# Performance work log

Measured on AMD Instinct MI355X. Metric: run time of the kernel, lower is better.

## Reference

```python
import jax, jax.numpy as jnp
import numpy as np

D_MODEL = 1024
HEADS = 4
DK = 1024          # key_dim = d_model * expand_k
DV = 2048          # value_dim = d_model * expand_v
HDK = DK // HEADS  # 256
HDV = DV // HEADS  # 512
LOW_RANK = 16
CHUNK = 64
GATE_NORM = 16.0
EPS = 1e-5


def setup_inputs() -> dict:
    key = jax.random.key(0)
    ks = jax.random.split(key, 10)
    gain = 2.0 ** (-2.5)

    def xavier(k, shape):  # shape = (fan_in, fan_out); stored as [in, out]
        lim = gain * np.sqrt(6.0 / (shape[0] + shape[1]))
        return jax.random.uniform(k, shape, jnp.float32, -lim, lim)

    return {
        'x': jax.random.normal(ks[0], (2, 2048, D_MODEL), jnp.float32),
        'Wq': xavier(ks[1], (D_MODEL, DK)),
        'Wk': xavier(ks[2], (D_MODEL, DK)),
        'Wv': xavier(ks[3], (D_MODEL, DV)),
        'Wg': xavier(ks[4], (D_MODEL, DV)),
        'Wgk1': xavier(ks[5], (D_MODEL, LOW_RANK)),
        'Wgk2': xavier(ks[6], (LOW_RANK, DK)),
        'bgk2': jnp.zeros((DK,), jnp.float32),
        'Wo': xavier(ks[7], (DV, D_MODEL)),
        'rms_w': jnp.ones((HDV,), jnp.float32),
    }


def _gla_chunked(q, k, v, g):
    """Gated linear attention: S_t = exp(g_t) (*) S_{t-1} + k_t^T v_t;  o_t = scale * q_t @ S_t.
    q,k,g: [B,H,T,HDK]; v: [B,H,T,HDV]. Chunk-parallel formulation, scan over chunks."""
    B, H, T, _ = q.shape
    NC = T // CHUNK
    scale = HDK ** -0.5

    def to_chunks(t, d):  # [B,H,T,d] -> [NC,B,H,CHUNK,d]
        return t.reshape(B, H, NC, CHUNK, d).transpose(2, 0, 1, 3, 4)

    qc = to_chunks(q, HDK)
    kc = to_chunks(k, HDK)
    vc = to_chunks(v, HDV)
    bc = jnp.cumsum(to_chunks(g, HDK), axis=-2)  # inclusive log-decay within chunk
    mask = jnp.tril(jnp.ones((CHUNK, CHUNK), bool))

    def step(S, inp):
        qb, kb, vb, bb = inp                       # [B,H,C,HDK/HDV]
        qg = qb * jnp.exp(bb) * scale              # queries decayed to chunk start
        kd = kb * jnp.exp(-bb)                     # keys un-decayed (intra)
        A = jnp.einsum('bhtd,bhsd->bhts', qg, kd)  # intra-chunk scores
        A = jnp.where(mask, A, 0.0)
        o = jnp.einsum('bhts,bhsv->bhtv', A, vb) + jnp.einsum('bhtd,bhdv->bhtv', qg, S)
        b_last = bb[:, :, -1:, :]                  # [B,H,1,HDK]
        kg = kb * jnp.exp(b_last - bb)             # keys decayed to chunk end
        S = S * jnp.exp(b_last[:, :, 0, :])[..., None] + jnp.einsum('bhtd,bhtv->bhdv', kg, vb)
        return S, o

    S0 = jnp.zeros((B, H, HDK, HDV), q.dtype)
    _, o = jax.lax.scan(step, S0, (qc, kc, vc, bc))  # o: [NC,B,H,C,HDV]
    return o.transpose(1, 2, 0, 3, 4).reshape(B, H, T, HDV)


def reference(x, Wq, Wk, Wv, Wg, Wgk1, Wgk2, bgk2, Wo, rms_w):
    B, T, _ = x.shape
    q = (x @ Wq).reshape(B, T, HEADS, HDK).transpose(0, 2, 1, 3)
    k = (x @ Wk).reshape(B, T, HEADS, HDK).transpose(0, 2, 1, 3)
    v = (x @ Wv).reshape(B, T, HEADS, HDV).transpose(0, 2, 1, 3)
    gk = (x @ Wgk1) @ Wgk2 + bgk2                       # low-rank gate logits
    g = jax.nn.log_sigmoid(gk.astype(jnp.float32)) / GATE_NORM
    g = g.reshape(B, T, HEADS, HDK).transpose(0, 2, 1, 3)

    o = _gla_chunked(q, k, v, g)                        # [B,H,T,HDV]
    o = o.transpose(0, 2, 1, 3)                         # [B,T,H,HDV]
    o = o * jax.lax.rsqrt(jnp.mean(o * o, axis=-1, keepdims=True) + EPS) * rms_w
    o = o.reshape(B, T, HEADS * HDV)
    o = o * jax.nn.silu(x @ Wg)
    return o @ Wo
```

## Files before the change

### kernel.cpp

```cpp
#include <hip/hip_runtime.h>
#include <hip/hip_bf16.h>
#include <math.h>

#define TOK  4096
#define DM   1024
#define DKC  1024
#define DVC  2048
#define NH   4
#define HDK_ 256
#define HDV_ 512
#define NCH  32
#define CHK  64

typedef __attribute__((ext_vector_type(8))) short bf16x8;
typedef __attribute__((ext_vector_type(4))) float f32x4;

__device__ inline float bf2f(short s) {
    unsigned int b = ((unsigned int)(unsigned short)s) << 16;
    return __uint_as_float(b);
}
__device__ inline short f2bf_bits(float f) {
    __hip_bfloat16 h = __float2bfloat16(f);
    return *reinterpret_cast<short*>(&h);
}

__device__ __forceinline__ void gl_lds16(const void* g, void* l) {
    __builtin_amdgcn_global_load_lds((const __attribute__((address_space(1))) void*)g,
                                     (__attribute__((address_space(3))) void*)l, 16, 0, 0);
}

__global__ __launch_bounds__(256) void prep_all(const float* __restrict__ Wq,
                                                const float* __restrict__ Wk,
                                                const float* __restrict__ Wv,
                                                const float* __restrict__ Wg,
                                                const float* __restrict__ Wo,
                                                __hip_bfloat16* __restrict__ WtAll,
                                                __hip_bfloat16* __restrict__ WtO,
                                                const float* __restrict__ x,
                                                const float* __restrict__ W1,
                                                const float* __restrict__ W2,
                                                const float* __restrict__ b2,
                                                __hip_bfloat16* __restrict__ xb,
                                                float* __restrict__ g) {
    const int bid = blockIdx.x;
    const int tid = threadIdx.x;
    if (bid < 8192) {
        __shared__ float tile[32][33];
        const float* W; __hip_bfloat16* Wt; int K, N, r;
        if (bid < 1024)      { W = Wq; Wt = WtAll;               K = 1024; N = 1024; r = bid; }
        else if (bid < 2048) { W = Wk; Wt = WtAll + 1024 * 1024; K = 1024; N = 1024; r = bid - 1024; }
        else if (bid < 4096) { W = Wv; Wt = WtAll + 2048 * 1024; K = 1024; N = 2048; r = bid - 2048; }
        else if (bid < 6144) { W = Wg; Wt = WtAll + 4096 * 1024; K = 1024; N = 2048; r = bid - 4096; }
        else                 { W = Wo; Wt = WtO;                 K = 2048; N = 1024; r = bid - 6144; }
        const int ncols = N >> 5;
        const int n0 = (r % ncols) * 32, k0 = (r / ncols) * 32;
        const int tx = tid & 31, ty = tid >> 5;
#pragma unroll
        for (int i = 0; i < 32; i += 8)
            tile[ty + i][tx] = W[(size_t)(k0 + ty + i) * N + n0 + tx];
        __syncthreads();
#pragma unroll
        for (int i = 0; i < 32; i += 8)
            Wt[(size_t)(n0 + ty + i) * K + k0 + tx] = __float2bfloat16(tile[tx][ty + i]);
    } else {
        __shared__ float xl[1024];
        __shared__ float red[16][17];
        __shared__ float t1l[16];
        const int t = bid - 8192;
        float4 xv = *reinterpret_cast<const float4*>(&x[(size_t)t * DM + tid * 4]);
        *reinterpret_cast<float4*>(&xl[tid * 4]) = xv;
        short4 xs;
        xs.x = f2bf_bits(xv.x); xs.y = f2bf_bits(xv.y);
        xs.z = f2bf_bits(xv.z); xs.w = f2bf_bits(xv.w);
        *reinterpret_cast<short4*>((short*)xb + (size_t)t * DM + tid * 4) = xs;
        __syncthreads();
        const int o = tid & 15, p = tid >> 4;
        float s = 0.f;
#pragma unroll 8
        for (int m = 0; m < 64; ++m) {
            int kk = p * 64 + m;
            s += xl[kk] * W1[kk * 16 + o];
        }
        red[p][o] = s;
        __syncthreads();
        if (tid < 16) {
            float tot = 0.f;
#pragma unroll
            for (int pp = 0; pp < 16; ++pp) tot += red[pp][tid];
            t1l[tid] = tot;
        }
        __syncthreads();
#pragma unroll
        for (int j = 0; j < 4; ++j) {
            int c = tid + j * 256;
            float acc = b2[c];
#pragma unroll
            for (int r2 = 0; r2 < 16; ++r2) acc += t1l[r2] * W2[r2 * 1024 + c];
            float ls = fminf(acc, 0.f) - log1pf(expf(-fabsf(acc)));
            g[(size_t)t * DKC + c] = ls * (1.f / 16.f);
        }
    }
}

__global__ __launch_bounds__(512) void gemm256(const __hip_bfloat16* __restrict__ A,
                                               const __hip_bfloat16* __restrict__ Wt,
                                               __hip_bfloat16* __restrict__ qo,
                                               __hip_bfloat16* __restrict__ ko,
                                               __hip_bfloat16* __restrict__ vT,
                                               __hip_bfloat16* __restrict__ xgo) {
    __shared__ __align__(16) short SM[9 * 8192];
    const int K = 1024, NT = 16;
    const int tid = threadIdx.x;
    const int wave = tid >> 6, lane = tid & 63;
    const int wr = wave >> 2;
    const int wc = wave & 3;
    const int hc = wc >> 1;
    const int l15 = lane & 15, kb = lane >> 4;
    const int m0 = blockIdx.y * 128, n0 = blockIdx.x * 256;

    const bool isV = (n0 >= 2048 && n0 < 4096);
    __hip_bfloat16* dst = nullptr; int ldd = 0, nloc0 = 0;
    if (n0 < 1024)       { dst = qo;  ldd = 1024; nloc0 = n0; }
    else if (n0 < 2048)  { dst = ko;  ldd = 1024; nloc0 = n0 - 1024; }
    else if (n0 >= 4096) { dst = xgo; ldd = 2048; nloc0 = n0 - 4096; }

    f32x4 acc[4][4];
#pragma unroll
    for (int mf = 0; mf < 4; ++mf)
#pragma unroll
        for (int nf = 0; nf < 4; ++nf) acc[mf][nf] = (f32x4){0.f, 0.f, 0.f, 0.f};

    auto stage_unit = [&](int u) {
        int tk = u / 3, p = u % 3;
        int slot = u % 9;
#pragma unroll
        for (int j = 0; j < 2; ++j) {
            int row = (wave * 2 + j) * 8 + (lane >> 3);
            int srcg = (lane & 7) ^ (row & 7);
            const __hip_bfloat16* src =
                (p == 0) ? &A[(size_t)(m0 + row) * K + tk * 64 + srcg * 8]
                         : &Wt[(size_t)(n0 + (p - 1) * 128 + row) * K + tk * 64 + srcg * 8];
            gl_lds16(src, &SM[slot * 8192 + (wave * 2 + j) * 512]);
        }
    };

    for (int u = 0; u <= 5; ++u) stage_unit(u);

    const int ULAST = 3 * NT - 1;
    for (int t = 0; t < NT; ++t) {
        if (t < NT - 1) asm volatile("s_waitcnt vmcnt(6)" ::: "memory");
        else            asm volatile("s_waitcnt vmcnt(0)" ::: "memory");
        __builtin_amdgcn_sched_barrier(0);
        __builtin_amdgcn_s_barrier();

        if (3 * t + 6 <= ULAST) stage_unit(3 * t + 6);
        if (3 * t + 7 <= ULAST) stage_unit(3 * t + 7);
        if (3 * t + 8 <= ULAST) stage_unit(3 * t + 8);
        __builtin_amdgcn_sched_barrier(0);

        const short* Abase = &SM[((3 * t) % 9) * 8192];
        const short* Bbase = &SM[((3 * t + 1 + hc) % 9) * 8192];

        bf16x8 a0[4], b0[4], a1[4], b1[4];
#pragma unroll
        for (int mf = 0; mf < 4; ++mf) {
            int row = wr * 64 + mf * 16 + l15;
            a0[mf] = *reinterpret_cast<const bf16x8*>(&Abase[row * 64 + (kb ^ (row & 7)) * 8]);
        }
#pragma unroll
        for (int nf = 0; nf < 4; ++nf) {
            int row = (wc & 1) * 64 + nf * 16 + l15;
            b0[nf] = *reinterpret_cast<const bf16x8*>(&Bbase[row * 64 + (kb ^ (row & 7)) * 8]);
        }
        __builtin_amdgcn_sched_barrier(0);
#pragma unroll
        for (int mf = 0; mf < 4; ++mf) {
            int row = wr * 64 + mf * 16 + l15;
            a1[mf] = *reinterpret_cast<const bf16x8*>(&Abase[row * 64 + ((4 + kb) ^ (row & 7)) * 8]);
        }
#pragma unroll
        for (int nf = 0; nf < 4; ++nf) {
            int row = (wc & 1) * 64 + nf * 16 + l15;
            b1[nf] = *reinterpret_cast<const bf16x8*>(&Bbase[row * 64 + ((4 + kb) ^ (row & 7)) * 8]);
        }
        __builtin_amdgcn_sched_barrier(0);
        asm volatile("s_waitcnt lgkmcnt(8)" ::: "memory");
        __builtin_amdgcn_sched_barrier(0);
        __builtin_amdgcn_s_setprio(1);
#pragma unroll
        for (int mf = 0; mf < 4; ++mf)
#pragma unroll
            for (int nf = 0; nf < 4; ++nf)
                acc[mf][nf] = __builtin_amdgcn_mfma_f32_16x16x32_bf16(a0[mf], b0[nf], acc[mf][nf], 0, 0, 0);
        __builtin_amdgcn_s_setprio(0);
        asm volatile("s_waitcnt lgkmcnt(0)" ::: "memory");
        __builtin_amdgcn_sched_barrier(0);
        __builtin_amdgcn_s_setprio(1);
#pragma unroll
        for (int mf = 0; mf < 4; ++mf)
#pragma unroll
            for (int nf = 0; nf < 4; ++nf)
                acc[mf][nf] = __builtin_amdgcn_mfma_f32_16x16x32_bf16(a1[mf], b1[nf], acc[mf][nf], 0, 0, 0);
        __builtin_amdgcn_s_setprio(0);
    }

    if (!isV) {
#pragma unroll
        for (int mf = 0; mf < 4; ++mf)
#pragma unroll
            for (int nf = 0; nf < 4; ++nf)
#pragma unroll
                for (int r = 0; r < 4; ++r)
                    dst[(size_t)(m0 + wr * 64 + mf * 16 + kb * 4 + r) * ldd +
                        nloc0 + wc * 64 + nf * 16 + l15] = __float2bfloat16(acc[mf][nf][r]);
    } else {
        __syncthreads();
        short* Cl = SM;
#pragma unroll
        for (int mf = 0; mf < 4; ++mf)
#pragma unroll
            for (int nf = 0; nf < 4; ++nf)
#pragma unroll
                for (int r = 0; r < 4; ++r) {
                    int trow = wr * 64 + mf * 16 + kb * 4 + r;
                    int vcol = wc * 64 + nf * 16 + l15;
                    Cl[vcol * 132 + trow] = f2bf_bits(acc[mf][nf][r]);
                }
        __syncthreads();
        const int vcg0 = n0 - 2048;
        const int bh = (m0 >> 11) * NH + (vcg0 >> 9);
        const int vl0 = vcg0 & 511;
        const int tl0 = m0 & 2047;
        short* vTs = (short*)vT;
#pragma unroll
        for (int it = 0; it < 8; ++it) {
            int idx = tid + it * 512;
            int row = idx >> 4;
            int c8 = (idx & 15) * 8;
            bf16x8 vv = *reinterpret_cast<const bf16x8*>(&Cl[row * 132 + c8]);
            *reinterpret_cast<bf16x8*>(
                &vTs[((size_t)(bh * 512 + vl0 + row)) * 2048 + tl0 + c8]) = vv;
        }
    }
}

__global__ __launch_bounds__(256) void gemm_bf16(const __hip_bfloat16* __restrict__ A,
                                                 const __hip_bfloat16* __restrict__ Wt,
                                                 float* __restrict__ C,
                                                 int M, int N, int K) {
    __shared__ __align__(16) short Buf[2][2][128 * 64];
    const int tid = threadIdx.x;
    const int wave = tid >> 6, lane = tid & 63;
    const int wr = wave >> 1, wc = wave & 1;
    const int m0 = blockIdx.y * 128, n0 = blockIdx.x * 128;
    const int l15 = lane & 15, kb = lane >> 4;
    const int lr8 = lane >> 3, lc8 = (lane & 7) * 8;
    const int NT = K >> 6;

    f32x4 acc[4][4];
#pragma unroll
    for (int mf = 0; mf < 4; ++mf)
#pragma unroll
        for (int nf = 0; nf < 4; ++nf) acc[mf][nf] = (f32x4){0.f, 0.f, 0.f, 0.f};

#define STAGE_G(kt, bi)                                                          \
    {                                                                            \
        int k0s = (kt) * 64;                                                     \
        _Pragma("unroll")                                                        \
        for (int j = 0; j < 4; ++j) {                                            \
            int inst = wave * 4 + j;                                             \
            int r = inst * 8 + lr8;                                              \
            gl_lds16(&A[(size_t)(m0 + r) * K + k0s + lc8], &Buf[bi][0][inst * 512]); \
            gl_lds16(&Wt[(size_t)(n0 + r) * K + k0s + lc8], &Buf[bi][1][inst * 512]); \
        }                                                                        \
    }

    STAGE_G(0, 0);
    STAGE_G(1, 1);

    for (int t = 0; t < NT; ++t) {
        if (t + 1 < NT) asm volatile("s_waitcnt vmcnt(8)" ::: "memory");
        else            asm volatile("s_waitcnt vmcnt(0)" ::: "memory");
        __builtin_amdgcn_sched_barrier(0);
        __builtin_amdgcn_s_barrier();
        const short* Ab = Buf[t & 1][0];
        const short* Bb = Buf[t & 1][1];
        bf16x8 a0[4], b0[4], a1[4], b1[4];
#pragma unroll
        for (int mf = 0; mf < 4; ++mf)
            a0[mf] = *reinterpret_cast<const bf16x8*>(&Ab[(wr * 64 + mf * 16 + l15) * 64 + kb * 8]);
#pragma unroll
        for (int nf = 0; nf < 4; ++nf)
            b0[nf] = *reinterpret_cast<const bf16x8*>(&Bb[(wc * 64 + nf * 16 + l15) * 64 + kb * 8]);
        __builtin_amdgcn_sched_barrier(0);
#pragma unroll
        for (int mf = 0; mf < 4; ++mf)
            a1[mf] = *reinterpret_cast<const bf16x8*>(&Ab[(wr * 64 + mf * 16 + l15) * 64 + 32 + kb * 8]);
#pragma unroll
        for (int nf = 0; nf < 4; ++nf)
            b1[nf] = *reinterpret_cast<const bf16x8*>(&Bb[(wc * 64 + nf * 16 + l15) * 64 + 32 + kb * 8]);
        __builtin_amdgcn_sched_barrier(0);
        asm volatile("s_waitcnt lgkmcnt(8)" ::: "memory");
        __builtin_amdgcn_sched_barrier(0);
#pragma unroll
        for (int mf = 0; mf < 4; ++mf)
#pragma unroll
            for (int nf = 0; nf < 4; ++nf)
                acc[mf][nf] = __builtin_amdgcn_mfma_f32_16x16x32_bf16(a0[mf], b0[nf], acc[mf][nf], 0, 0, 0);
        asm volatile("s_waitcnt lgkmcnt(0)" ::: "memory");
        __builtin_amdgcn_sched_barrier(0);
#pragma unroll
        for (int mf = 0; mf < 4; ++mf)
#pragma unroll
            for (int nf = 0; nf < 4; ++nf)
                acc[mf][nf] = __builtin_amdgcn_mfma_f32_16x16x32_bf16(a1[mf], b1[nf], acc[mf][nf], 0, 0, 0);
        __builtin_amdgcn_sched_barrier(0);
        __builtin_amdgcn_s_barrier();
        if (t + 2 < NT) STAGE_G(t + 2, t & 1);
    }
#undef STAGE_G

#pragma unroll
    for (int mf = 0; mf < 4; ++mf)
#pragma unroll
        for (int nf = 0; nf < 4; ++nf)
#pragma unroll
            for (int r = 0; r < 4; ++r)
                C[(size_t)(m0 + wr * 64 + mf * 16 + kb * 4 + r) * N + n0 + wc * 64 + nf * 16 + l15] =
                    acc[mf][nf][r];
}

__global__ __launch_bounds__(256) void gla_chunk(const __hip_bfloat16* __restrict__ qb,
                                                 const __hip_bfloat16* __restrict__ kb,
                                                 const __hip_bfloat16* __restrict__ vT,
                                                 const float* __restrict__ g,
                                                 __hip_bfloat16* __restrict__ qg,
                                                 __hip_bfloat16* __restrict__ kgT,
                                                 __hip_bfloat16* __restrict__ o1,
                                                 float* __restrict__ dlast) {
    __shared__ __align__(16) short SM[36864];
    short* qg_l = SM;
    short* kd_l = SM + 16384;
    short* V_l  = SM;
    short* Am_l = SM + 32768;

    const int chunk = blockIdx.x, bh = blockIdx.y;
    const int b = bh >> 2, h = bh & 3;
    const int t0 = b * 2048 + chunk * 64;
    const int tt0 = chunk * 64;
    const int tid = threadIdx.x;
    const float scale = 0.0625f;

    {
        const int d = tid;
        const float* gcol = g + (size_t)t0 * DKC + h * HDK_ + d;
        const __hip_bfloat16* qcol = qb + (size_t)t0 * DKC + h * HDK_ + d;
        const __hip_bfloat16* kcol = kb + (size_t)t0 * DKC + h * HDK_ + d;
        float run = 0.f;
#pragma unroll
        for (int i = 0; i < 64; ++i) run += gcol[(size_t)i * DKC];
        const float ebl = expf(run);
        dlast[((size_t)bh * NCH + chunk) * HDK_ + d] = ebl;

        bf16x8 kreg[8];
        run = 0.f;
#pragma unroll
        for (int i = 0; i < 64; ++i) {
            run += gcol[(size_t)i * DKC];
            float eb = expf(run);
            float qv = __bfloat162float(qcol[(size_t)i * DKC]) * eb * scale;
            float kdv = __bfloat162float(kcol[(size_t)i * DKC]) * expf(-run);
            qg[(size_t)(t0 + i) * DKC + h * HDK_ + d] = __float2bfloat16(qv);
            int bq = ((i * 512 + d * 2) ^ ((i & 7) << 4)) >> 1;
            qg_l[bq] = f2bf_bits(qv);
            kd_l[bq] = f2bf_bits(kdv);
            kreg[i >> 3][i & 7] = f2bf_bits(kdv * ebl);
        }
        __hip_bfloat16* kdst = kgT + ((size_t)(bh * HDK_ + d)) * 2048 + chunk * 64;
#pragma unroll
        for (int j = 0; j < 8; ++j)
            *reinterpret_cast<bf16x8*>(&kdst[j * 8]) = kreg[j];
    }
    __syncthreads();

    const int wv = tid >> 6, lane = tid & 63;
    const int l15 = lane & 15, kb_ = lane >> 4;

    {
        f32x4 accA[4];
#pragma unroll
        for (int sf = 0; sf < 4; ++sf) accA[sf] = (f32x4){0.f, 0.f, 0.f, 0.f};
        const int trow = wv * 16 + l15;
#pragma unroll
        for (int ks = 0; ks < 8; ++ks) {
            bf16x8 af = *reinterpret_cast<const bf16x8*>(
                &qg_l[((trow * 512 + (ks * 32 + kb_ * 8) * 2) ^ ((trow & 7) << 4)) >> 1]);
#pragma unroll
            for (int sf = 0; sf < 4; ++sf) {
                int srow = sf * 16 + l15;
                bf16x8 bfr = *reinterpret_cast<const bf16x8*>(
                    &kd_l[((srow * 512 + (ks * 32 + kb_ * 8) * 2) ^ ((srow & 7) << 4)) >> 1]);
                accA[sf] = __builtin_amdgcn_mfma_f32_16x16x32_bf16(af, bfr, accA[sf], 0, 0, 0);
            }
        }
#pragma unroll
        for (int sf = 0; sf < 4; ++sf)
#pragma unroll
            for (int r = 0; r < 4; ++r) {
                int t = wv * 16 + kb_ * 4 + r, s = sf * 16 + l15;
                float val = (t >= s) ? accA[sf][r] : 0.f;
                Am_l[((t * 128 + s * 2) ^ ((t & 7) << 4)) >> 1] = f2bf_bits(val);
            }
    }
    __syncthreads();

    {
        const int lr8 = lane >> 3, slot = lane & 7;
#pragma unroll
        for (int i8 = 0; i8 < 16; ++i8) {
            int vrow0 = wv * 128 + i8 * 8;
            const __hip_bfloat16* src =
                &vT[((size_t)bh * 512 + vrow0 + lr8) * 2048 + tt0 + (slot ^ (lr8 & 7)) * 8];
            gl_lds16(src, &V_l[vrow0 * 64]);
        }
    }
    __syncthreads();

    {
        f32x4 accO[4][8];
#pragma unroll
        for (int tf = 0; tf < 4; ++tf)
#pragma unroll
            for (int vf = 0; vf < 8; ++vf) accO[tf][vf] = (f32x4){0.f, 0.f, 0.f, 0.f};
#pragma unroll
        for (int kk = 0; kk < 2; ++kk) {
            bf16x8 af[4];
#pragma unroll
            for (int tf = 0; tf < 4; ++tf) {
                int row = tf * 16 + l15;
                af[tf] = *reinterpret_cast<const bf16x8*>(
                    &Am_l[((row * 128 + (kk * 32 + kb_ * 8) * 2) ^ ((row & 7) << 4)) >> 1]);
            }
#pragma unroll
            for (int vf = 0; vf < 8; ++vf) {
                int rv = wv * 128 + vf * 16 + l15;
                bf16x8 bfr = *reinterpret_cast<const bf16x8*>(
                    &V_l[((rv * 128 + (kk * 32 + kb_ * 8) * 2) ^ ((rv & 7) << 4)) >> 1]);
#pragma unroll
                for (int tf = 0; tf < 4; ++tf)
                    accO[tf][vf] = __builtin_amdgcn_mfma_f32_16x16x32_bf16(af[tf], bfr, accO[tf][vf], 0, 0, 0);
            }
        }
#pragma unroll
        for (int tf = 0; tf < 4; ++tf)
#pragma unroll
            for (int vf = 0; vf < 8; ++vf)
#pragma unroll
                for (int r = 0; r < 4; ++r) {
                    int t = tf * 16 + kb_ * 4 + r;
                    int vv = wv * 128 + vf * 16 + l15;
                    o1[(size_t)(t0 + t) * DVC + h * HDV_ + vv] = __float2bfloat16(accO[tf][vf][r]);
                }
    }
}

__global__ __launch_bounds__(256) void u_pass(const __hip_bfloat16* __restrict__ vT,
                                              const __hip_bfloat16* __restrict__ kgT,
                                              __hip_bfloat16* __restrict__ U) {
    __shared__ __align__(16) short Av[128 * 64];
    __shared__ __align__(16) short Bv[128 * 64];
    const int bx = blockIdx.x, c = blockIdx.y, bh = blockIdx.z;
    const int vc0 = (bx >> 1) * 128, d0 = (bx & 1) * 128;
    const int tid = threadIdx.x;
    const int wave = tid >> 6, lane = tid & 63;
    const int wr = wave >> 1, wc = wave & 1;
    const int l15 = lane & 15, kb = lane >> 4;
    const int lr8 = lane >> 3, lc8 = (lane & 7) * 8;

#pragma unroll
    for (int j = 0; j < 4; ++j) {
        int inst = wave * 4 + j;
        int r = inst * 8 + lr8;
        gl_lds16(&vT[((size_t)bh * 512 + vc0 + r) * 2048 + c * 64 + lc8], &Av[inst * 512]);
        gl_lds16(&kgT[((size_t)bh * HDK_ + d0 + r) * 2048 + c * 64 + lc8], &Bv[inst * 512]);
    }
    __syncthreads();

    f32x4 acc[4][4];
#pragma unroll
    for (int mf = 0; mf < 4; ++mf)
#pragma unroll
        for (int nf = 0; nf < 4; ++nf) acc[mf][nf] = (f32x4){0.f, 0.f, 0.f, 0.f};
#pragma unroll
    for (int kk = 0; kk < 2; ++kk) {
        bf16x8 af[4], bfr[4];
#pragma unroll
        for (int mf = 0; mf < 4; ++mf)
            af[mf] = *reinterpret_cast<const bf16x8*>(&Av[(wr * 64 + mf * 16 + l15) * 64 + kk * 32 + kb * 8]);
#pragma unroll
        for (int nf = 0; nf < 4; ++nf)
            bfr[nf] = *reinterpret_cast<const bf16x8*>(&Bv[(wc * 64 + nf * 16 + l15) * 64 + kk * 32 + kb * 8]);
#pragma unroll
        for (int mf = 0; mf < 4; ++mf)
#pragma unroll
            for (int nf = 0; nf < 4; ++nf)
                acc[mf][nf] = __builtin_amdgcn_mfma_f32_16x16x32_bf16(af[mf], bfr[nf], acc[mf][nf], 0, 0, 0);
    }
    const size_t Ub = ((size_t)bh * NCH + c) * 131072;
#pragma unroll
    for (int mf = 0; mf < 4; ++mf)
#pragma unroll
        for (int nf = 0; nf < 4; ++nf)
#pragma unroll
            for (int r = 0; r < 4; ++r) {
                int vc = vc0 + wr * 64 + mf * 16 + kb * 4 + r;
                int d = d0 + wc * 64 + nf * 16 + l15;
                U[Ub + (size_t)vc * 256 + d] = __float2bfloat16(acc[mf][nf][r]);
            }
}

__global__ __launch_bounds__(256) void scan_pass(__hip_bfloat16* __restrict__ U,
                                                 const float* __restrict__ dlast) {
    int gid = blockIdx.x * 256 + threadIdx.x;
    int bh = gid >> 14;
    int rem = gid & 16383;
    int vc = rem >> 5;
    int dg = rem & 31;
    float S[8];
#pragma unroll
    for (int j = 0; j < 8; ++j) S[j] = 0.f;
    size_t base = (size_t)bh * NCH * 131072 + (size_t)vc * 256 + dg * 8;
    for (int c = 0; c < NCH; ++c) {
        __hip_bfloat16* p = U + base + (size_t)c * 131072;
        bf16x8 u = *reinterpret_cast<bf16x8*>(p);
        const float* dl = &dlast[((size_t)bh * NCH + c) * HDK_ + dg * 8];
        float4 e0 = *reinterpret_cast<const float4*>(dl);
        float4 e1 = *reinterpret_cast<const float4*>(dl + 4);
        float e[8] = {e0.x, e0.y, e0.z, e0.w, e1.x, e1.y, e1.z, e1.w};
        bf16x8 outv;
#pragma unroll
        for (int j = 0; j < 8; ++j) {
            outv[j] = f2bf_bits(S[j]);
            S[j] = S[j] * e[j] + bf2f(u[j]);
        }
        *reinterpret_cast<bf16x8*>(p) = outv;
    }
}

__global__ __launch_bounds__(256) void o_pass(const __hip_bfloat16* __restrict__ qg,
                                              const __hip_bfloat16* __restrict__ U,
                                              const __hip_bfloat16* __restrict__ o1,
                                              __hip_bfloat16* __restrict__ o2) {
    __shared__ __align__(16) char smem[64 * 132 * 4];
    short* Av = (short*)smem;
    short* Bv = (short*)smem + 128 * 64;
    float* oT = (float*)smem;
    const int vt = blockIdx.x, c = blockIdx.y, bh = blockIdx.z;
    const int b = bh >> 2, h = bh & 3;
    const int vc0 = vt * 128;
    const int t0 = b * 2048 + c * 64;
    const int tid = threadIdx.x;
    const int wave = tid >> 6, lane = tid & 63;
    const int wr = wave >> 1, wc = wave & 1;
    const int l15 = lane & 15, kb = lane >> 4;
    const int lr8 = lane >> 3, lc8 = (lane & 7) * 8;
    const size_t Ub = ((size_t)bh * NCH + c) * 131072;

    f32x4 acc[4][2];
#pragma unroll
    for (int mf = 0; mf < 4; ++mf)
#pragma unroll
        for (int nf = 0; nf < 2; ++nf) acc[mf][nf] = (f32x4){0.f, 0.f, 0.f, 0.f};

    for (int ks = 0; ks < 4; ++ks) {
        const int d0 = ks * 64;
#pragma unroll
        for (int j = 0; j < 4; ++j) {
            int inst = wave * 4 + j;
            int r = inst * 8 + lr8;
            gl_lds16(&U[Ub + (size_t)(vc0 + r) * 256 + d0 + lc8], &Av[inst * 512]);
        }
#pragma unroll
        for (int j = 0; j < 2; ++j) {
            int inst = wave * 2 + j;
            int r = inst * 8 + lr8;
            gl_lds16(&qg[(size_t)(t0 + r) * DKC + h * HDK_ + d0 + lc8], &Bv[inst * 512]);
        }
        __syncthreads();
#pragma unroll
        for (int kk = 0; kk < 2; ++kk) {
            bf16x8 af[4], bfr[2];
#pragma unroll
            for (int mf = 0; mf < 4; ++mf)
                af[mf] = *reinterpret_cast<const bf16x8*>(&Av[(wr * 64 + mf * 16 + l15) * 64 + kk * 32 + kb * 8]);
#pragma unroll
            for (int nf = 0; nf < 2; ++nf)
                bfr[nf] = *reinterpret_cast<const bf16x8*>(&Bv[(wc * 32 + nf * 16 + l15) * 64 + kk * 32 + kb * 8]);
#pragma unroll
            for (int mf = 0; mf < 4; ++mf)
#pragma unroll
                for (int nf = 0; nf < 2; ++nf)
                    acc[mf][nf] = __builtin_amdgcn_mfma_f32_16x16x32_bf16(af[mf], bfr[nf], acc[mf][nf], 0, 0, 0);
        }
        __syncthreads();
    }
#pragma unroll
    for (int mf = 0; mf < 4; ++mf)
#pragma unroll
        for (int nf = 0; nf < 2; ++nf)
#pragma unroll
            for (int r = 0; r < 4; ++r)
                oT[(wc * 32 + nf * 16 + l15) * 132 + wr * 64 + mf * 16 + kb * 4 + r] = acc[mf][nf][r];
    __syncthreads();
#pragma unroll
    for (int j = 0; j < 4; ++j) {
        int t = (tid >> 4) + j * 16;
        int vc8 = (tid & 15) * 8;
        float4 a0 = *reinterpret_cast<const float4*>(&oT[t * 132 + vc8]);
        float4 a1 = *reinterpret_cast<const float4*>(&oT[t * 132 + vc8 + 4]);
        size_t oi = (size_t)(t0 + t) * DVC + h * HDV_ + vc0 + vc8;
        bf16x8 iv = *reinterpret_cast<const bf16x8*>(&o1[oi]);
        bf16x8 outv;
        outv[0] = f2bf_bits(a0.x + bf2f(iv[0]));
        outv[1] = f2bf_bits(a0.y + bf2f(iv[1]));
        outv[2] = f2bf_bits(a0.z + bf2f(iv[2]));
        outv[3] = f2bf_bits(a0.w + bf2f(iv[3]));
        outv[4] = f2bf_bits(a1.x + bf2f(iv[4]));
        outv[5] = f2bf_bits(a1.y + bf2f(iv[5]));
        outv[6] = f2bf_bits(a1.z + bf2f(iv[6]));
        outv[7] = f2bf_bits(a1.w + bf2f(iv[7]));
        *reinterpret_cast<bf16x8*>((__hip_bfloat16*)o2 + oi) = outv;
    }
}

__global__ __launch_bounds__(256) void rms_gate(const __hip_bfloat16* __restrict__ o2,
                                                const __hip_bfloat16* __restrict__ xg,
                                                const float* __restrict__ rms_w,
                                                __hip_bfloat16* __restrict__ gated) {
    __shared__ float wsum[4];
    const int th = blockIdx.x;
    const int t = th >> 2, h = th & 3;
    const int tid = threadIdx.x;
    const size_t base = (size_t)t * DVC + h * HDV_;
    short2 ov = reinterpret_cast<const short2*>((const short*)o2 + base)[tid];
    float v0 = bf2f(ov.x), v1 = bf2f(ov.y);
    float s = v0 * v0 + v1 * v1;
#pragma unroll
    for (int off = 32; off >= 1; off >>= 1) s += __shfl_down(s, off, 64);
    if ((tid & 63) == 0) wsum[tid >> 6] = s;
    __syncthreads();
    float tot = wsum[0] + wsum[1] + wsum[2] + wsum[3];
    float rms = rsqrtf(tot * (1.f / 512.f) + 1e-5f);
    short2 gv = reinterpret_cast<const short2*>((const short*)xg + base)[tid];
    float g0 = bf2f(gv.x), g1 = bf2f(gv.y);
    float s0 = g0 / (1.f + expf(-g0));
    float s1 = g1 / (1.f + expf(-g1));
    float2 w = reinterpret_cast<const float2*>(rms_w)[tid];
    short2 outp;
    outp.x = f2bf_bits(v0 * rms * w.x * s0);
    outp.y = f2bf_bits(v1 * rms * w.y * s1);
    reinterpret_cast<short2*>((short*)gated + base)[tid] = outp;
}

extern "C" void kernel_launch(void* const* d_in, const int* in_sizes, int n_in,
                              void* d_out, int out_size, void* d_ws, size_t ws_size,
                              hipStream_t stream) {
    const float* x    = (const float*)d_in[0];
    const float* Wq   = (const float*)d_in[1];
    const float* Wk   = (const float*)d_in[2];
    const float* Wv   = (const float*)d_in[3];
    const float* Wg   = (const float*)d_in[4];
    const float* Wgk1 = (const float*)d_in[5];
    const float* Wgk2 = (const float*)d_in[6];
    const float* bgk2 = (const float*)d_in[7];
    const float* Wo   = (const float*)d_in[8];
    const float* rmsw = (const float*)d_in[9];
    float* out = (float*)d_out;
    float* ws = (float*)d_ws;

    const size_t M1 = 1ull << 20;
    __hip_bfloat16* xb    = (__hip_bfloat16*)ws;
    __hip_bfloat16* WtAll = (__hip_bfloat16*)(ws + 2 * M1);
    __hip_bfloat16* q_b   = (__hip_bfloat16*)(ws + 5 * M1);
    __hip_bfloat16* k_b   = (__hip_bfloat16*)(ws + 7 * M1);
    float*          g     = ws + 13 * M1;
    __hip_bfloat16* U     = (__hip_bfloat16*)ws;
    __hip_bfloat16* xg_b  = (__hip_bfloat16*)(ws + 17 * M1);
    __hip_bfloat16* qgb   = (__hip_bfloat16*)(ws + 21 * M1);
    __hip_bfloat16* kgT   = (__hip_bfloat16*)(ws + 23 * M1);
    __hip_bfloat16* vT    = (__hip_bfloat16*)(ws + 25 * M1);
    __hip_bfloat16* o1    = (__hip_bfloat16*)(ws + 29 * M1);
    __hip_bfloat16* o2    = (__hip_bfloat16*)(ws + 33 * M1);
    float*          dlast = ws + 37 * M1 + 65536;
    __hip_bfloat16* WtO   = (__hip_bfloat16*)(ws + 38 * M1);
    __hip_bfloat16* gated = (__hip_bfloat16*)(ws + 25 * M1);

    prep_all<<<12288, 256, 0, stream>>>(Wq, Wk, Wv, Wg, Wo, WtAll, WtO,
                                        x, Wgk1, Wgk2, bgk2, xb, g);

    gemm256<<<dim3(24, 32), 512, 0, stream>>>(xb, WtAll, q_b, k_b, vT, xg_b);

    gla_chunk<<<dim3(NCH, 8), 256, 0, stream>>>(q_b, k_b, vT, g, qgb, kgT, o1, dlast);

    u_pass<<<dim3(8, NCH, 8), 256, 0, stream>>>(vT, kgT, U);
    scan_pass<<<512, 256, 0, stream>>>(U, dlast);
    o_pass<<<dim3(4, NCH, 8), 256, 0, stream>>>(qgb, U, o1, o2);

    rms_gate<<<TOK * NH, 256, 0, stream>>>(o2, xg_b, rmsw, gated);
    gemm_bf16<<<dim3(8, 32), 256, 0, stream>>>(gated, WtO, out, TOK, DM, DVC);
}
```

Baseline: 238.0 us.

## Fuse chunk state-update GEMM into gla_chunk and drop kgT round-trip

```diff
diff --git a/kernel.cpp b/kernel.cpp
--- a/kernel.cpp
+++ b/kernel.cpp
@@ -335,14 +335,15 @@
                                                  const __hip_bfloat16* __restrict__ vT,
                                                  const float* __restrict__ g,
                                                  __hip_bfloat16* __restrict__ qg,
-                                                 __hip_bfloat16* __restrict__ kgT,
+                                                 __hip_bfloat16* __restrict__ U,
                                                  __hip_bfloat16* __restrict__ o1,
                                                  float* __restrict__ dlast) {
-    __shared__ __align__(16) short SM[36864];
+    __shared__ __align__(16) short SM[53248];
     short* qg_l = SM;
     short* kd_l = SM + 16384;
     short* V_l  = SM;
-    short* Am_l = SM + 32768;
+    short* kg_l = SM + 32768;
+    short* Am_l = SM + 49152;
 
     const int chunk = blockIdx.x, bh = blockIdx.y;
     const int b = bh >> 2, h = bh & 3;
@@ -376,10 +377,9 @@
             kd_l[bq] = f2bf_bits(kdv);
             kreg[i >> 3][i & 7] = f2bf_bits(kdv * ebl);
         }
-        __hip_bfloat16* kdst = kgT + ((size_t)(bh * HDK_ + d)) * 2048 + chunk * 64;
 #pragma unroll
         for (int j = 0; j < 8; ++j)
-            *reinterpret_cast<bf16x8*>(&kdst[j * 8]) = kreg[j];
+            *reinterpret_cast<bf16x8*>(&kg_l[d * 64 + ((j ^ (d & 7)) * 8)]) = kreg[j];
     }
     __syncthreads();
 
@@ -462,61 +462,48 @@
                     o1[(size_t)(t0 + t) * DVC + h * HDV_ + vv] = __float2bfloat16(accO[tf][vf][r]);
                 }
     }
-}
-
-__global__ __launch_bounds__(256) void u_pass(const __hip_bfloat16* __restrict__ vT,
-                                              const __hip_bfloat16* __restrict__ kgT,
-                                              __hip_bfloat16* __restrict__ U) {
-    __shared__ __align__(16) short Av[128 * 64];
-    __shared__ __align__(16) short Bv[128 * 64];
-    const int bx = blockIdx.x, c = blockIdx.y, bh = blockIdx.z;
-    const int vc0 = (bx >> 1) * 128, d0 = (bx & 1) * 128;
-    const int tid = threadIdx.x;
-    const int wave = tid >> 6, lane = tid & 63;
-    const int wr = wave >> 1, wc = wave & 1;
-    const int l15 = lane & 15, kb = lane >> 4;
-    const int lr8 = lane >> 3, lc8 = (lane & 7) * 8;
-
-#pragma unroll
-    for (int j = 0; j < 4; ++j) {
-        int inst = wave * 4 + j;
-        int r = inst * 8 + lr8;
-        gl_lds16(&vT[((size_t)bh * 512 + vc0 + r) * 2048 + c * 64 + lc8], &Av[inst * 512]);
-        gl_lds16(&kgT[((size_t)bh * HDK_ + d0 + r) * 2048 + c * 64 + lc8], &Bv[inst * 512]);
-    }
-    __syncthreads();
-
-    f32x4 acc[4][4];
-#pragma unroll
-    for (int mf = 0; mf < 4; ++mf)
-#pragma unroll
-        for (int nf = 0; nf < 4; ++nf) acc[mf][nf] = (f32x4){0.f, 0.f, 0.f, 0.f};
-#pragma unroll
-    for (int kk = 0; kk < 2; ++kk) {
-        bf16x8 af[4], bfr[4];
-#pragma unroll
-        for (int mf = 0; mf < 4; ++mf)
-            af[mf] = *reinterpret_cast<const bf16x8*>(&Av[(wr * 64 + mf * 16 + l15) * 64 + kk * 32 + kb * 8]);
-#pragma unroll
-        for (int nf = 0; nf < 4; ++nf)
-            bfr[nf] = *reinterpret_cast<const bf16x8*>(&Bv[(wc * 64 + nf * 16 + l15) * 64 + kk * 32 + kb * 8]);
-#pragma unroll
-        for (int mf = 0; mf < 4; ++mf)
-#pragma unroll
-            for (int nf = 0; nf < 4; ++nf)
-                acc[mf][nf] = __builtin_amdgcn_mfma_f32_16x16x32_bf16(af[mf], bfr[nf], acc[mf][nf], 0, 0, 0);
-    }
-    const size_t Ub = ((size_t)bh * NCH + c) * 131072;
-#pragma unroll
-    for (int mf = 0; mf < 4; ++mf)
-#pragma unroll
-        for (int nf = 0; nf < 4; ++nf)
-#pragma unroll
-            for (int r = 0; r < 4; ++r) {
-                int vc = vc0 + wr * 64 + mf * 16 + kb * 4 + r;
-                int d = d0 + wc * 64 + nf * 16 + l15;
-                U[Ub + (size_t)vc * 256 + d] = __float2bfloat16(acc[mf][nf][r]);
+
+    {
+        const size_t Ub = ((size_t)bh * NCH + chunk) * 131072;
+        for (int d0 = 0; d0 < 256; d0 += 64) {
+            f32x4 accU[8][4];
+#pragma unroll
+            for (int vf = 0; vf < 8; ++vf)
+#pragma unroll
+                for (int nf = 0; nf < 4; ++nf) accU[vf][nf] = (f32x4){0.f, 0.f, 0.f, 0.f};
+#pragma unroll
+            for (int kk = 0; kk < 2; ++kk) {
+                bf16x8 av[8], bv[4];
+#pragma unroll
+                for (int vf = 0; vf < 8; ++vf) {
+                    int rv = wv * 128 + vf * 16 + l15;
+                    av[vf] = *reinterpret_cast<const bf16x8*>(
+                        &V_l[((rv * 128 + (kk * 32 + kb_ * 8) * 2) ^ ((rv & 7) << 4)) >> 1]);
+                }
+#pragma unroll
+                for (int nf = 0; nf < 4; ++nf) {
+                    int row = d0 + nf * 16 + l15;
+                    bv[nf] = *reinterpret_cast<const bf16x8*>(
+                        &kg_l[row * 64 + (((kk * 4 + kb_) ^ (row & 7)) * 8)]);
+                }
+#pragma unroll
+                for (int vf = 0; vf < 8; ++vf)
+#pragma unroll
+                    for (int nf = 0; nf < 4; ++nf)
+                        accU[vf][nf] = __builtin_amdgcn_mfma_f32_16x16x32_bf16(av[vf], bv[nf], accU[vf][nf], 0, 0, 0);
             }
+#pragma unroll
+            for (int vf = 0; vf < 8; ++vf)
+#pragma unroll
+                for (int nf = 0; nf < 4; ++nf)
+#pragma unroll
+                    for (int r = 0; r < 4; ++r) {
+                        int vc = wv * 128 + vf * 16 + kb_ * 4 + r;
+                        int d = d0 + nf * 16 + l15;
+                        U[Ub + (size_t)vc * 256 + d] = __float2bfloat16(accU[vf][nf][r]);
+                    }
+        }
+    }
 }
 
 __global__ __launch_bounds__(256) void scan_pass(__hip_bfloat16* __restrict__ U,
@@ -687,7 +674,6 @@
     __hip_bfloat16* U     = (__hip_bfloat16*)ws;
     __hip_bfloat16* xg_b  = (__hip_bfloat16*)(ws + 17 * M1);
     __hip_bfloat16* qgb   = (__hip_bfloat16*)(ws + 21 * M1);
-    __hip_bfloat16* kgT   = (__hip_bfloat16*)(ws + 23 * M1);
     __hip_bfloat16* vT    = (__hip_bfloat16*)(ws + 25 * M1);
     __hip_bfloat16* o1    = (__hip_bfloat16*)(ws + 29 * M1);
     __hip_bfloat16* o2    = (__hip_bfloat16*)(ws + 33 * M1);
@@ -700,9 +686,8 @@
 
     gemm256<<<dim3(24, 32), 512, 0, stream>>>(xb, WtAll, q_b, k_b, vT, xg_b);
 
-    gla_chunk<<<dim3(NCH, 8), 256, 0, stream>>>(q_b, k_b, vT, g, qgb, kgT, o1, dlast);
-
-    u_pass<<<dim3(8, NCH, 8), 256, 0, stream>>>(vT, kgT, U);
+    gla_chunk<<<dim3(NCH, 8), 256, 0, stream>>>(q_b, k_b, vT, g, qgb, U, o1, dlast);
+
     scan_pass<<<512, 256, 0, stream>>>(U, dlast);
     o_pass<<<dim3(4, NCH, 8), 256, 0, stream>>>(qgb, U, o1, o2);
 
```

After: 224.5 us. -5.7%, faster.
